# Performance work log

Measured on AMD Instinct MI355X. Metric: run time of the kernel, lower is better.

Reference implementation:

```python
import jax, jax.numpy as jnp
import numpy as np

B, T, D = 4, 2048, 1024
H, DH = 16, 64

def setup_inputs() -> dict:
    key = jax.random.key(0)
    k1, k2, k3 = jax.random.split(key, 3)
    x = jax.random.normal(k1, (B, T, D), dtype=jnp.float32)
    # nn.Linear weights stored [out, in]; we keep that convention
    w_attn = jax.random.normal(k2, (3 * D, D), dtype=jnp.float32) * (1.0 / np.sqrt(D))
    w_proj = jax.random.normal(k3, (D, D), dtype=jnp.float32) * (1.0 / np.sqrt(D))
    return {"x": x, "w_attn": w_attn, "w_proj": w_proj}

def reference(x, w_attn, w_proj):
    Bx, Tx, Dx = x.shape
    qkv = jnp.einsum('btd,ed->bte', x, w_attn)            # [B,T,3D]
    qkv = qkv.reshape(Bx, Tx, 3, H, DH)
    q = qkv[:, :, 0].transpose(0, 2, 1, 3)                # [B,H,T,DH]
    k = qkv[:, :, 1].transpose(0, 2, 1, 3)
    v = qkv[:, :, 2].transpose(0, 2, 1, 3)
    scale = 1.0 / np.sqrt(DH).astype(np.float32)
    att = jnp.einsum('bhqd,bhkd->bhqk', q, k) * scale     # [B,H,T,T]
    causal = jnp.tril(jnp.ones((Tx, Tx), dtype=bool))
    att = jnp.where(causal[None, None], att, jnp.float32(-jnp.inf))
    att = jax.nn.softmax(att, axis=-1)
    y = jnp.einsum('bhqk,bhkd->bhqd', att, v)             # [B,H,T,DH]
    y = y.transpose(0, 2, 1, 3).reshape(Bx, Tx, Dx)       # [B,T,D]
    y = jnp.einsum('btd,ed->bte', y, w_proj)
    return y
```

## Files before the change

kernel.cpp:

```cpp
#include <hip/hip_runtime.h>

typedef unsigned short u16;
typedef __bf16 bf16x8 __attribute__((ext_vector_type(8)));
typedef float floatx4 __attribute__((ext_vector_type(4)));

__device__ inline u16 f2bf(float x) {
    unsigned int u = __builtin_bit_cast(unsigned int, x);
    return (u16)((u + 0x7FFFu + ((u >> 16) & 1u)) >> 16);
}

__device__ inline floatx4 fzero() {
    floatx4 z = {0.f, 0.f, 0.f, 0.f};
    return z;
}

#if defined(__has_builtin)
#if __has_builtin(__builtin_amdgcn_exp2f)
#define EXP2F(x) __builtin_amdgcn_exp2f(x)
#endif
#endif
#ifndef EXP2F
#define EXP2F(x) exp2f(x)
#endif

template <bool F32>
__device__ inline bf16x8 ld8(const void* base, size_t off) {
    if constexpr (F32) {
        const float* p = (const float*)base + off;
        float4 a = *(const float4*)p;
        float4 b = *(const float4*)(p + 4);
        union { u16 u[8]; bf16x8 v; } t;
        t.u[0] = f2bf(a.x); t.u[1] = f2bf(a.y); t.u[2] = f2bf(a.z); t.u[3] = f2bf(a.w);
        t.u[4] = f2bf(b.x); t.u[5] = f2bf(b.y); t.u[6] = f2bf(b.z); t.u[7] = f2bf(b.w);
        return t.v;
    } else {
        return *(const bf16x8*)((const u16*)base + off);
    }
}

__global__ __launch_bounds__(256) void cvt_f32_bf16(const float* __restrict__ src,
                                                    u16* __restrict__ dst, int n8) {
    int i = blockIdx.x * 256 + threadIdx.x;
    if (i >= n8) return;
    dst += (size_t)i * 8;
    *(bf16x8*)dst = ld8<true>(src, (size_t)i * 8);
}

#define BK 32

template <bool AF32, bool BF32, bool CF32>
__global__ __launch_bounds__(256) void gemm_bt(const void* __restrict__ Ap,
                                               const void* __restrict__ Bp,
                                               void* __restrict__ Cp,
                                               int M, int N, int K) {
    __shared__ alignas(16) u16 As[128 * BK];
    __shared__ alignas(16) u16 Bs[128 * BK];

    const int tid  = threadIdx.x;
    const int lane = tid & 63;
    const int wave = tid >> 6;
    const int wm = (wave >> 1) * 64;
    const int wn = (wave & 1) * 64;
    const int tm = blockIdx.y * 128;
    const int tn = blockIdx.x * 128;
    const int l15 = lane & 15;
    const int l4  = lane >> 4;

    const int srow = tid >> 2;
    const int scol = (tid & 3) * 8;

    floatx4 acc[4][4];
#pragma unroll
    for (int i = 0; i < 4; i++)
#pragma unroll
        for (int j = 0; j < 4; j++) acc[i][j] = fzero();

    for (int k0 = 0; k0 < K; k0 += BK) {
        bf16x8 av[2], bv[2];
#pragma unroll
        for (int q = 0; q < 2; q++) {
            av[q] = ld8<AF32>(Ap, (size_t)(tm + srow + q * 64) * K + k0 + scol);
            bv[q] = ld8<BF32>(Bp, (size_t)(tn + srow + q * 64) * K + k0 + scol);
        }
        __syncthreads();
#pragma unroll
        for (int q = 0; q < 2; q++) {
            *(bf16x8*)&As[(srow + q * 64) * BK + scol] = av[q];
            *(bf16x8*)&Bs[(srow + q * 64) * BK + scol] = bv[q];
        }
        __syncthreads();

        bf16x8 af[4], bf[4];
#pragma unroll
        for (int i = 0; i < 4; i++)
            af[i] = *(const bf16x8*)&As[(wm + i * 16 + l15) * BK + l4 * 8];
#pragma unroll
        for (int j = 0; j < 4; j++)
            bf[j] = *(const bf16x8*)&Bs[(wn + j * 16 + l15) * BK + l4 * 8];
#pragma unroll
        for (int i = 0; i < 4; i++)
#pragma unroll
            for (int j = 0; j < 4; j++)
                acc[i][j] = __builtin_amdgcn_mfma_f32_16x16x32_bf16(af[i], bf[j], acc[i][j], 0, 0, 0);
    }

#pragma unroll
    for (int i = 0; i < 4; i++)
#pragma unroll
        for (int j = 0; j < 4; j++)
#pragma unroll
            for (int r = 0; r < 4; r++) {
                int row = tm + wm + i * 16 + l4 * 4 + r;
                int col = tn + wn + j * 16 + l15;
                if constexpr (CF32)
                    ((float*)Cp)[(size_t)row * N + col] = acc[i][j][r];
                else
                    ((u16*)Cp)[(size_t)row * N + col] = f2bf(acc[i][j][r]);
            }
}

__global__ __launch_bounds__(256) void transpose_v(const u16* __restrict__ qkv,
                                                   u16* __restrict__ vT) {
    __shared__ alignas(16) u16 Ts[64 * 80];
    const int bh = blockIdx.x;
    const int b = bh >> 4, h = bh & 15;
    const int t0 = blockIdx.y * 64;
    const int tid = threadIdx.x;
    const int r = tid >> 3;
    const int c = tid & 7;
#pragma unroll
    for (int p = 0; p < 2; p++) {
        int tr = r + p * 32;
        *(bf16x8*)&Ts[tr * 80 + c * 8] =
            *(const bf16x8*)&qkv[(size_t)(b * 2048 + t0 + tr) * 3072 + 2048 + h * 64 + c * 8];
    }
    __syncthreads();
#pragma unroll
    for (int p = 0; p < 2; p++) {
        int dr = r + p * 32;
        union { u16 u[8]; bf16x8 v; } t;
#pragma unroll
        for (int i = 0; i < 8; i++) t.u[i] = Ts[(c * 8 + i) * 80 + dr];
        *(bf16x8*)&vT[(size_t)bh * 131072 + (size_t)dr * 2048 + t0 + c * 8] = t.v;
    }
}

#define AST 88

template <bool USE_VT>
__global__ __launch_bounds__(256) void attn2(const u16* __restrict__ qkv,
                                             const u16* __restrict__ vT,
                                             u16* __restrict__ y) {
    const int T = 2048, CW = 3072;
    __shared__ alignas(16) u16 KP[64 * AST];
    __shared__ alignas(16) u16 Vt[64 * AST];

    const int tid  = threadIdx.x;
    const int lane = tid & 63;
    const int wave = tid >> 6;
    const int l15 = lane & 15;
    const int l4  = lane >> 4;

    const int bh = blockIdx.x;
    const int qt = 31 - blockIdx.y;
    const int b = bh >> 4, h = bh & 15;
    const int q0 = qt * 64;

    const size_t base = (size_t)b * T * CW + h * 64;
    const u16* qp = qkv + base;
    const u16* kp = qkv + base + 1024;
    const u16* vp = qkv + base + 2048;
    const u16* vtp = USE_VT ? (vT + (size_t)bh * 131072) : nullptr;

    bf16x8 qf[2];
    {
        int qrow = q0 + wave * 16 + l15;
        qf[0] = *(const bf16x8*)&qp[(size_t)qrow * CW + l4 * 8];
        qf[1] = *(const bf16x8*)&qp[(size_t)qrow * CW + 32 + l4 * 8];
    }

    const float C2 = 0.18033688f;
    float lrow[4] = {0.f, 0.f, 0.f, 0.f};
    floatx4 Oacc[4];
#pragma unroll
    for (int cf = 0; cf < 4; cf++) Oacc[cf] = fzero();

    const int sr = tid >> 3;
    const int sc = tid & 7;

    for (int kt = 0; kt <= qt; kt++) {
        const int t0 = kt * 64;
        __syncthreads();

#pragma unroll
        for (int p = 0; p < 2; p++) {
            int tr = sr + p * 32;
            *(bf16x8*)&KP[tr * AST + sc * 8] =
                *(const bf16x8*)&kp[(size_t)(t0 + tr) * CW + sc * 8];
        }
        if constexpr (USE_VT) {
#pragma unroll
            for (int p = 0; p < 2; p++) {
                int dr = sr + p * 32;
                *(bf16x8*)&Vt[dr * AST + sc * 8] =
                    *(const bf16x8*)&vtp[(size_t)dr * 2048 + t0 + sc * 8];
            }
        } else {
            int dh = tid & 63;
            int tb = (tid >> 6) * 8;
#pragma unroll
            for (int p = 0; p < 2; p++) {
                int tl = tb + p * 32;
                union { u16 u[8]; bf16x8 v; } tmp;
#pragma unroll
                for (int i = 0; i < 8; i++)
                    tmp.u[i] = vp[(size_t)(t0 + tl + i) * CW + dh];
                *(bf16x8*)&Vt[dh * AST + tl] = tmp.v;
            }
        }
        __syncthreads();

        floatx4 sfr[4];
#pragma unroll
        for (int j = 0; j < 4; j++) {
            bf16x8 k0f = *(const bf16x8*)&KP[(j * 16 + l15) * AST + l4 * 8];
            bf16x8 k1f = *(const bf16x8*)&KP[(j * 16 + l15) * AST + 32 + l4 * 8];
            floatx4 s = fzero();
            s = __builtin_amdgcn_mfma_f32_16x16x32_bf16(qf[0], k0f, s, 0, 0, 0);
            s = __builtin_amdgcn_mfma_f32_16x16x32_bf16(qf[1], k1f, s, 0, 0, 0);
            sfr[j] = s;
        }
        bf16x8 v0f[4], v1f[4];
#pragma unroll
        for (int cf = 0; cf < 4; cf++) {
            v0f[cf] = *(const bf16x8*)&Vt[(cf * 16 + l15) * AST + l4 * 8];
            v1f[cf] = *(const bf16x8*)&Vt[(cf * 16 + l15) * AST + 32 + l4 * 8];
        }

        float pj[4][4];
        if (kt == qt) {
#pragma unroll
            for (int j = 0; j < 4; j++)
#pragma unroll
                for (int r = 0; r < 4; r++) {
                    int qrow = q0 + wave * 16 + l4 * 4 + r;
                    int krow = t0 + j * 16 + l15;
                    float e = (krow <= qrow) ? sfr[j][r] * C2 : -1.0e30f;
                    pj[j][r] = EXP2F(e);
                }
        } else {
#pragma unroll
            for (int j = 0; j < 4; j++)
#pragma unroll
                for (int r = 0; r < 4; r++)
                    pj[j][r] = EXP2F(sfr[j][r] * C2);
        }
#pragma unroll
        for (int r = 0; r < 4; r++)
            lrow[r] += (pj[0][r] + pj[1][r]) + (pj[2][r] + pj[3][r]);

        __syncthreads();
#pragma unroll
        for (int j = 0; j < 4; j++)
#pragma unroll
            for (int r = 0; r < 4; r++)
                KP[(wave * 16 + l4 * 4 + r) * AST + j * 16 + l15] = f2bf(pj[j][r]);
        __syncthreads();

        bf16x8 pf0 = *(const bf16x8*)&KP[(wave * 16 + l15) * AST + l4 * 8];
        bf16x8 pf1 = *(const bf16x8*)&KP[(wave * 16 + l15) * AST + 32 + l4 * 8];
#pragma unroll
        for (int cf = 0; cf < 4; cf++) {
            Oacc[cf] = __builtin_amdgcn_mfma_f32_16x16x32_bf16(pf0, v0f[cf], Oacc[cf], 0, 0, 0);
            Oacc[cf] = __builtin_amdgcn_mfma_f32_16x16x32_bf16(pf1, v1f[cf], Oacc[cf], 0, 0, 0);
        }
    }

#pragma unroll
    for (int r = 0; r < 4; r++) {
#pragma unroll
        for (int off = 1; off < 16; off <<= 1)
            lrow[r] += __shfl_xor(lrow[r], off, 64);
    }
#pragma unroll
    for (int r = 0; r < 4; r++) {
        float inv = 1.0f / lrow[r];
        int qrow = q0 + wave * 16 + l4 * 4 + r;
        size_t orow = ((size_t)b * T + qrow) * 1024 + h * 64;
#pragma unroll
        for (int cf = 0; cf < 4; cf++)
            y[orow + cf * 16 + l15] = f2bf(Oacc[cf][r] * inv);
    }
}

extern "C" void kernel_launch(void* const* d_in, const int* in_sizes, int n_in,
                              void* d_out, int out_size, void* d_ws, size_t ws_size,
                              hipStream_t stream) {
    const float* x      = (const float*)d_in[0];
    const float* w_attn = (const float*)d_in[1];
    const float* w_proj = (const float*)d_in[2];
    float* out = (float*)d_out;

    const size_t QKV = (size_t)8192 * 3072;
    const size_t Y   = (size_t)8192 * 1024;
    const size_t VTE = (size_t)64 * 64 * 2048;
    const size_t XB  = (size_t)8192 * 1024;
    const size_t WAB = (size_t)3072 * 1024;
    const size_t WPB = (size_t)1024 * 1024;

    u16* qkv = (u16*)d_ws;
    u16* yb  = qkv + QKV;

    const bool full = ws_size >= (QKV + Y + VTE + XB + WAB + WPB) * sizeof(u16);
    const bool mid  = ws_size >= (QKV + Y + VTE) * sizeof(u16);
    if (ws_size < (QKV + Y) * sizeof(u16)) return;

    dim3 blk(256);
    dim3 g1(3072 / 128, 8192 / 128), g2(1024 / 128, 8192 / 128);
    dim3 ga(64, 32);

    if (full) {
        u16* vT  = yb + Y;
        u16* xb  = vT + VTE;
        u16* wab = xb + XB;
        u16* wpb = wab + WAB;
        cvt_f32_bf16<<<(XB / 8 + 255) / 256, blk, 0, stream>>>(x, xb, (int)(XB / 8));
        cvt_f32_bf16<<<(WAB / 8 + 255) / 256, blk, 0, stream>>>(w_attn, wab, (int)(WAB / 8));
        cvt_f32_bf16<<<(WPB / 8 + 255) / 256, blk, 0, stream>>>(w_proj, wpb, (int)(WPB / 8));
        gemm_bt<false, false, false><<<g1, blk, 0, stream>>>(xb, wab, qkv, 8192, 3072, 1024);
        transpose_v<<<ga, blk, 0, stream>>>(qkv, vT);
        attn2<true><<<ga, blk, 0, stream>>>(qkv, vT, yb);
        gemm_bt<false, false, true><<<g2, blk, 0, stream>>>(yb, wpb, out, 8192, 1024, 1024);
    } else if (mid) {
        u16* vT = yb + Y;
        gemm_bt<true, true, false><<<g1, blk, 0, stream>>>(x, w_attn, qkv, 8192, 3072, 1024);
        transpose_v<<<ga, blk, 0, stream>>>(qkv, vT);
        attn2<true><<<ga, blk, 0, stream>>>(qkv, vT, yb);
        gemm_bt<false, true, true><<<g2, blk, 0, stream>>>(yb, w_proj, out, 8192, 1024, 1024);
    } else {
        gemm_bt<true, true, false><<<g1, blk, 0, stream>>>(x, w_attn, qkv, 8192, 3072, 1024);
        attn2<false><<<ga, blk, 0, stream>>>(qkv, nullptr, yb);
        gemm_bt<false, true, true><<<g2, blk, 0, stream>>>(yb, w_proj, out, 8192, 1024, 1024);
    }
}
```

Before: 281.3 us.

## Use direct global-to-LDS loads in GEMM and pipeline attention K/V tiles with swizzled LDS

For bf16 inputs, the GEMM now loads tiles with global_load_lds, writing straight from global memory into shared memory without staging through registers. The attention kernel prefetches the next K/V tile into registers while the current tile is computed. It also replaces the padded LDS layout with an XOR swizzle and gives P its own buffer, which removes two barriers per iteration. The direct-to-LDS path relies on the per-wave LDS placement matching the As/Bs layout, and the wave-private P buffer is now written and read without a barrier.

```diff
diff --git a/kernel.cpp b/kernel.cpp
--- a/kernel.cpp
+++ b/kernel.cpp
@@ -38,6 +38,16 @@
     }
 }
 
+typedef __attribute__((address_space(1))) const unsigned int as1_u32;
+typedef __attribute__((address_space(3))) unsigned int as3_u32;
+__device__ inline void gld_lds16(const void* g, void* l) {
+    __builtin_amdgcn_global_load_lds((as1_u32*)g, (as3_u32*)l, 16, 0, 0);
+}
+
+__device__ inline u16* swz_ptr(u16* buf, int row, int col) {
+    return (u16*)((char*)buf + row * 128 + ((col * 2) ^ ((row & 7) << 4)));
+}
+
 __global__ __launch_bounds__(256) void cvt_f32_bf16(const float* __restrict__ src,
                                                     u16* __restrict__ dst, int n8) {
     int i = blockIdx.x * 256 + threadIdx.x;
@@ -75,20 +85,36 @@
 #pragma unroll
         for (int j = 0; j < 4; j++) acc[i][j] = fzero();
 
+    const u16* Ag = nullptr;
+    const u16* Bg = nullptr;
+    if constexpr (!AF32 && !BF32) {
+        Ag = (const u16*)Ap + (size_t)(tm + srow) * K + scol;
+        Bg = (const u16*)Bp + (size_t)(tn + srow) * K + scol;
+    }
+
     for (int k0 = 0; k0 < K; k0 += BK) {
-        bf16x8 av[2], bv[2];
-#pragma unroll
-        for (int q = 0; q < 2; q++) {
-            av[q] = ld8<AF32>(Ap, (size_t)(tm + srow + q * 64) * K + k0 + scol);
-            bv[q] = ld8<BF32>(Bp, (size_t)(tn + srow + q * 64) * K + k0 + scol);
-        }
-        __syncthreads();
-#pragma unroll
-        for (int q = 0; q < 2; q++) {
-            *(bf16x8*)&As[(srow + q * 64) * BK + scol] = av[q];
-            *(bf16x8*)&Bs[(srow + q * 64) * BK + scol] = bv[q];
-        }
-        __syncthreads();
+        if constexpr (!AF32 && !BF32) {
+            __syncthreads();
+            gld_lds16(Ag + k0,                 &As[wave * 512]);
+            gld_lds16(Ag + k0 + (size_t)64 * K, &As[2048 + wave * 512]);
+            gld_lds16(Bg + k0,                 &Bs[wave * 512]);
+            gld_lds16(Bg + k0 + (size_t)64 * K, &Bs[2048 + wave * 512]);
+            __syncthreads();
+        } else {
+            bf16x8 av[2], bv[2];
+#pragma unroll
+            for (int q = 0; q < 2; q++) {
+                av[q] = ld8<AF32>(Ap, (size_t)(tm + srow + q * 64) * K + k0 + scol);
+                bv[q] = ld8<BF32>(Bp, (size_t)(tn + srow + q * 64) * K + k0 + scol);
+            }
+            __syncthreads();
+#pragma unroll
+            for (int q = 0; q < 2; q++) {
+                *(bf16x8*)&As[(srow + q * 64) * BK + scol] = av[q];
+                *(bf16x8*)&Bs[(srow + q * 64) * BK + scol] = bv[q];
+            }
+            __syncthreads();
+        }
 
         bf16x8 af[4], bf[4];
 #pragma unroll
@@ -145,15 +171,14 @@
     }
 }
 
-#define AST 88
-
 template <bool USE_VT>
 __global__ __launch_bounds__(256) void attn2(const u16* __restrict__ qkv,
                                              const u16* __restrict__ vT,
                                              u16* __restrict__ y) {
     const int T = 2048, CW = 3072;
-    __shared__ alignas(16) u16 KP[64 * AST];
-    __shared__ alignas(16) u16 Vt[64 * AST];
+    __shared__ alignas(16) u16 KP[64 * 64];
+    __shared__ alignas(16) u16 Vt[64 * 64];
+    __shared__ alignas(16) u16 PB[64 * 64];
 
     const int tid  = threadIdx.x;
     const int lane = tid & 63;
@@ -188,91 +213,89 @@
     const int sr = tid >> 3;
     const int sc = tid & 7;
 
+    bf16x8 kreg[2], vreg[2];
+    auto stage_load = [&](int kt) {
+        const int t0 = kt * 64;
+#pragma unroll
+        for (int p = 0; p < 2; p++)
+            kreg[p] = *(const bf16x8*)&kp[(size_t)(t0 + sr + p * 32) * CW + sc * 8];
+        if constexpr (USE_VT) {
+#pragma unroll
+            for (int p = 0; p < 2; p++)
+                vreg[p] = *(const bf16x8*)&vtp[(size_t)(sr + p * 32) * 2048 + t0 + sc * 8];
+        } else {
+            const int dh = tid & 63;
+            const int tb = wave * 8;
+#pragma unroll
+            for (int p = 0; p < 2; p++) {
+                union { u16 u[8]; bf16x8 v; } tmp;
+#pragma unroll
+                for (int i = 0; i < 8; i++)
+                    tmp.u[i] = vp[(size_t)(t0 + tb + p * 32 + i) * CW + dh];
+                vreg[p] = tmp.v;
+            }
+        }
+    };
+
+    stage_load(0);
+
     for (int kt = 0; kt <= qt; kt++) {
         const int t0 = kt * 64;
         __syncthreads();
 
 #pragma unroll
-        for (int p = 0; p < 2; p++) {
-            int tr = sr + p * 32;
-            *(bf16x8*)&KP[tr * AST + sc * 8] =
-                *(const bf16x8*)&kp[(size_t)(t0 + tr) * CW + sc * 8];
-        }
+        for (int p = 0; p < 2; p++)
+            *(bf16x8*)swz_ptr(KP, sr + p * 32, sc * 8) = kreg[p];
         if constexpr (USE_VT) {
 #pragma unroll
-            for (int p = 0; p < 2; p++) {
-                int dr = sr + p * 32;
-                *(bf16x8*)&Vt[dr * AST + sc * 8] =
-                    *(const bf16x8*)&vtp[(size_t)dr * 2048 + t0 + sc * 8];
-            }
+            for (int p = 0; p < 2; p++)
+                *(bf16x8*)swz_ptr(Vt, sr + p * 32, sc * 8) = vreg[p];
         } else {
-            int dh = tid & 63;
-            int tb = (tid >> 6) * 8;
-#pragma unroll
-            for (int p = 0; p < 2; p++) {
-                int tl = tb + p * 32;
-                union { u16 u[8]; bf16x8 v; } tmp;
-#pragma unroll
-                for (int i = 0; i < 8; i++)
-                    tmp.u[i] = vp[(size_t)(t0 + tl + i) * CW + dh];
-                *(bf16x8*)&Vt[dh * AST + tl] = tmp.v;
-            }
+            const int dh = tid & 63;
+            const int tb = wave * 8;
+#pragma unroll
+            for (int p = 0; p < 2; p++)
+                *(bf16x8*)swz_ptr(Vt, dh, tb + p * 32) = vreg[p];
         }
         __syncthreads();
 
-        floatx4 sfr[4];
+        if (kt < qt) stage_load(kt + 1);
+
 #pragma unroll
         for (int j = 0; j < 4; j++) {
-            bf16x8 k0f = *(const bf16x8*)&KP[(j * 16 + l15) * AST + l4 * 8];
-            bf16x8 k1f = *(const bf16x8*)&KP[(j * 16 + l15) * AST + 32 + l4 * 8];
+            bf16x8 k0f = *(const bf16x8*)swz_ptr(KP, j * 16 + l15, l4 * 8);
+            bf16x8 k1f = *(const bf16x8*)swz_ptr(KP, j * 16 + l15, 32 + l4 * 8);
             floatx4 s = fzero();
             s = __builtin_amdgcn_mfma_f32_16x16x32_bf16(qf[0], k0f, s, 0, 0, 0);
             s = __builtin_amdgcn_mfma_f32_16x16x32_bf16(qf[1], k1f, s, 0, 0, 0);
-            sfr[j] = s;
-        }
-        bf16x8 v0f[4], v1f[4];
-#pragma unroll
-        for (int cf = 0; cf < 4; cf++) {
-            v0f[cf] = *(const bf16x8*)&Vt[(cf * 16 + l15) * AST + l4 * 8];
-            v1f[cf] = *(const bf16x8*)&Vt[(cf * 16 + l15) * AST + 32 + l4 * 8];
-        }
-
-        float pj[4][4];
-        if (kt == qt) {
-#pragma unroll
-            for (int j = 0; j < 4; j++)
+            float pj[4];
+            if (kt == qt) {
 #pragma unroll
                 for (int r = 0; r < 4; r++) {
                     int qrow = q0 + wave * 16 + l4 * 4 + r;
                     int krow = t0 + j * 16 + l15;
-                    float e = (krow <= qrow) ? sfr[j][r] * C2 : -1.0e30f;
-                    pj[j][r] = EXP2F(e);
+                    float e = (krow <= qrow) ? s[r] * C2 : -1.0e30f;
+                    pj[r] = EXP2F(e);
                 }
-        } else {
-#pragma unroll
-            for (int j = 0; j < 4; j++)
-#pragma unroll
-                for (int r = 0; r < 4; r++)
-                    pj[j][r] = EXP2F(sfr[j][r] * C2);
-        }
-#pragma unroll
-        for (int r = 0; r < 4; r++)
-            lrow[r] += (pj[0][r] + pj[1][r]) + (pj[2][r] + pj[3][r]);
-
-        __syncthreads();
-#pragma unroll
-        for (int j = 0; j < 4; j++)
+            } else {
+#pragma unroll
+                for (int r = 0; r < 4; r++) pj[r] = EXP2F(s[r] * C2);
+            }
+#pragma unroll
+            for (int r = 0; r < 4; r++) lrow[r] += pj[r];
 #pragma unroll
             for (int r = 0; r < 4; r++)
-                KP[(wave * 16 + l4 * 4 + r) * AST + j * 16 + l15] = f2bf(pj[j][r]);
-        __syncthreads();
-
-        bf16x8 pf0 = *(const bf16x8*)&KP[(wave * 16 + l15) * AST + l4 * 8];
-        bf16x8 pf1 = *(const bf16x8*)&KP[(wave * 16 + l15) * AST + 32 + l4 * 8];
+                *swz_ptr(PB, wave * 16 + l4 * 4 + r, j * 16 + l15) = f2bf(pj[r]);
+        }
+
+        bf16x8 pf0 = *(const bf16x8*)swz_ptr(PB, wave * 16 + l15, l4 * 8);
+        bf16x8 pf1 = *(const bf16x8*)swz_ptr(PB, wave * 16 + l15, 32 + l4 * 8);
 #pragma unroll
         for (int cf = 0; cf < 4; cf++) {
-            Oacc[cf] = __builtin_amdgcn_mfma_f32_16x16x32_bf16(pf0, v0f[cf], Oacc[cf], 0, 0, 0);
-            Oacc[cf] = __builtin_amdgcn_mfma_f32_16x16x32_bf16(pf1, v1f[cf], Oacc[cf], 0, 0, 0);
+            bf16x8 v0f = *(const bf16x8*)swz_ptr(Vt, cf * 16 + l15, l4 * 8);
+            bf16x8 v1f = *(const bf16x8*)swz_ptr(Vt, cf * 16 + l15, 32 + l4 * 8);
+            Oacc[cf] = __builtin_amdgcn_mfma_f32_16x16x32_bf16(pf0, v0f, Oacc[cf], 0, 0, 0);
+            Oacc[cf] = __builtin_amdgcn_mfma_f32_16x16x32_bf16(pf1, v1f, Oacc[cf], 0, 0, 0);
         }
     }
 
```

New measurement: 270.5 us. 3.8% less time.
